# Kernel optimization log

Hardware: AMD Instinct MI355X
Metric: run time of the kernel (lower is better)

The kernel has to match this reference:

```python
import jax, jax.numpy as jnp
import numpy as np

N_VERTS = 2562


def _uniform(key, shape, bound):
    return jax.random.uniform(key, shape, jnp.float32, -bound, bound)


def vert_align(feat, pos):
    # feat: [B,C,H,W]; pos: [B,N,3], xy in [-1,1] -> bilinear sample -> [B,N,C]
    B, C, H, W = feat.shape
    ft = jnp.transpose(feat, (0, 2, 3, 1))  # [B,H,W,C]
    x = (jnp.clip(pos[..., 0], -1.0, 1.0) + 1.0) * 0.5 * (W - 1)
    y = (jnp.clip(pos[..., 1], -1.0, 1.0) + 1.0) * 0.5 * (H - 1)
    x0 = jnp.floor(x)
    y0 = jnp.floor(y)
    x0i = x0.astype(jnp.int32)
    y0i = y0.astype(jnp.int32)
    x1i = jnp.minimum(x0i + 1, W - 1)
    y1i = jnp.minimum(y0i + 1, H - 1)
    wx = (x - x0)[..., None]
    wy = (y - y0)[..., None]
    b = jnp.arange(B)[:, None]
    f00 = ft[b, y0i, x0i]
    f01 = ft[b, y0i, x1i]
    f10 = ft[b, y1i, x0i]
    f11 = ft[b, y1i, x1i]
    return (f00 * (1 - wx) * (1 - wy) + f01 * wx * (1 - wy)
            + f10 * (1 - wx) * wy + f11 * wx * wy)


def graph_conv(x, adj, w0, w1):
    # relu(x @ w0 + adj @ (x @ w1))
    return jax.nn.relu(x @ w0 + jnp.einsum('bij,bjc->bic', adj, x @ w1))


def setup_inputs() -> dict:
    key = jax.random.key(0)
    ks = jax.random.split(key, 20)
    B, N = 8, N_VERTS
    inp = {
        'conv2_3': jax.random.normal(ks[0], (B, 256, 56, 56), jnp.float32),
        'conv3_4': jax.random.normal(ks[1], (B, 512, 28, 28), jnp.float32),
        'conv4_6': jax.random.normal(ks[2], (B, 1024, 14, 14), jnp.float32),
        'conv5_3': jax.random.normal(ks[3], (B, 2048, 7, 7), jnp.float32),
        # scaled so row sums are O(1), like a normalized dense adjacency
        'vertex_adjacency': jax.random.uniform(ks[4], (B, N, N), jnp.float32) * (2.0 / N),
        'vertex_positions': jax.random.uniform(ks[5], (B, N, 3), jnp.float32) * 2.0 - 1.0,
        'vertex_features': jax.random.normal(ks[6], (B, N, 128), jnp.float32),
    }
    # learned parameters (torch default / GraphConv uniform init)
    inp['w_lin0'] = _uniform(ks[7], (3840, 128), 1.0 / np.sqrt(3840))
    inp['b_lin0'] = _uniform(ks[8], (128,), 1.0 / np.sqrt(3840))
    inp['gc0_w0'] = _uniform(ks[9], (259, 131), 1.0 / np.sqrt(259))
    inp['gc0_w1'] = _uniform(ks[10], (259, 131), 1.0 / np.sqrt(259))
    inp['gc1_w0'] = _uniform(ks[11], (131, 128), 1.0 / np.sqrt(131))
    inp['gc1_w1'] = _uniform(ks[12], (131, 128), 1.0 / np.sqrt(131))
    inp['gc2_w0'] = _uniform(ks[13], (131, 128), 1.0 / np.sqrt(131))
    inp['gc2_w1'] = _uniform(ks[14], (131, 128), 1.0 / np.sqrt(131))
    inp['w_lin1'] = _uniform(ks[15], (128, 3), 1.0 / np.sqrt(128))
    inp['b_lin1'] = _uniform(ks[16], (3,), 1.0 / np.sqrt(128))
    return inp


def reference(conv2_3, conv3_4, conv4_6, conv5_3, vertex_adjacency,
              vertex_positions, vertex_features,
              w_lin0, b_lin0, gc0_w0, gc0_w1, gc1_w0, gc1_w1,
              gc2_w0, gc2_w1, w_lin1, b_lin1):
    verts = jnp.concatenate(
        [vert_align(f, vertex_positions)
         for f in (conv2_3, conv3_4, conv4_6, conv5_3)], axis=2)  # [B,N,3840]
    projected = verts @ w_lin0 + b_lin0                             # [B,N,128]
    vf = jnp.concatenate([vertex_features, vertex_positions, projected], axis=2)  # 259
    h = graph_conv(vf, vertex_adjacency, gc0_w0, gc0_w1)            # [B,N,131]
    h = jnp.concatenate([vertex_positions, h], axis=2)              # 134? no: 3+131=134 -- see note
    h = graph_conv(h[:, :, :131] if h.shape[2] != 131 else h, vertex_adjacency, gc1_w0, gc1_w1)
    h = jnp.concatenate([vertex_positions, h], axis=2)              # 131
    new_features = graph_conv(h, vertex_adjacency, gc2_w0, gc2_w1)  # [B,N,128]
    new_positions = vertex_positions + jnp.tanh(new_features @ w_lin1 + b_lin1)
    return new_positions, new_features
```

## Files before the change

kernel.cpp:

```cpp
#include <hip/hip_runtime.h>
#include <hip/hip_bf16.h>

typedef __attribute__((ext_vector_type(8))) short bf16x8;
typedef __attribute__((ext_vector_type(4))) float f32x4;
typedef __attribute__((ext_vector_type(2))) float f32x2;
typedef long long i64;

static __device__ __forceinline__ float bflo(unsigned v){ return __uint_as_float(v << 16); }
static __device__ __forceinline__ float bfhi(unsigned v){ return __uint_as_float(v & 0xffff0000u); }
static __device__ __forceinline__ unsigned short f2bf(float f){
  unsigned u = __float_as_uint(f);
  u += 0x7FFFu + ((u >> 16) & 1u);
  return (unsigned short)(u >> 16);
}
static __device__ __forceinline__ unsigned f2e4m3(float x){
  unsigned b = __float_as_uint(x);
  unsigned s = (b >> 31) << 7;
  b &= 0x7fffffffu;
  if (b >= 0x43e80000u) return s | 0x7eu;
  if (b < 0x3c800000u)
    return s | (unsigned)rintf(__uint_as_float(b) * 512.f);
  unsigned b2 = b + 0x7ffffu + ((b >> 20) & 1u);
  return s | (((b2 >> 23) - 120u) << 3) | ((b2 >> 20) & 7u);
}
static __device__ __forceinline__ void gload_lds16(const void* g, void* l){
  __builtin_amdgcn_global_load_lds((const __attribute__((address_space(1))) unsigned int*)g,
                                   (__attribute__((address_space(3))) unsigned int*)l, 16, 0, 0);
}

#define MFMA16(acc, a, b) (acc) = __builtin_amdgcn_mfma_f32_16x16x32_bf16((a),(b),(acc),0,0,0)
#define MFMA8(acc, a, b)  (acc) = __builtin_amdgcn_mfma_f32_16x16x32_fp8_fp8((a),(b),(acc),0,0,0)

#define NB    8
#define NVRT  2562
#define MP    2624
#define NRB2  82
#define NRB16 164
#define NKT8  21
#define KOCT  336
#define YO    ((size_t)KOCT*128*8)

#define G_B0 0ul
#define G_B1 3211264ul
#define G_B2 4014080ul
#define G_B3 4214784ul
#define G_TOT 4264960ul

struct PWArgs {
  const float* src[7];
  unsigned short* dst[7];
  int ksrc[7], nsrc[7];
};
__global__ void k_packw_all(PWArgs a)
{
  const int cb[8] = {0,491520,528384,565248,585728,606208,626688,647168};
  int g = blockIdx.x * 256 + threadIdx.x;
#pragma unroll
  for (int s = 0; s < 7; s++){
    if (g >= cb[s] && g < cb[s+1]){
      int li = g - cb[s];
      int k = li >> 7, c = li & 127;
      int ks = a.ksrc[s], ns = a.nsrc[s];
      float v = (k < ks) ? a.src[s][(size_t)k * ns + c] : 0.f;
      a.dst[s][((size_t)(k >> 3) * 128 + c) * 8 + (k & 7)] = f2bf(v);
    }
  }
}

__global__ __launch_bounds__(256) void k_gproj2(
    const float* __restrict__ c0m, const float* __restrict__ c1m,
    const float* __restrict__ c2m, const float* __restrict__ c3m,
    const unsigned short* __restrict__ wp,
    unsigned short* __restrict__ G)
{
  __shared__ f32x4 red[3][1024];
  int bx = blockIdx.x;
  int m, b, tile;
  if (bx < 784)      { m = 0; b = bx / 98;  tile = bx - b*98; }
  else if (bx < 984) { int l = bx-784;  m = 1; b = l / 25; tile = l - b*25; }
  else if (bx < 1040){ int l = bx-984;  m = 2; b = l / 7;  tile = l - b*7; }
  else               { int l = bx-1040; m = 3; b = l >> 1; tile = l & 1; }
  int C  = 256 << m;
  int HW = (m==0)?3136:(m==1)?784:(m==2)?196:49;
  const float* src = ((m==0)?c0m:(m==1)?c1m:(m==2)?c2m:c3m) + (size_t)b * C * HW;
  size_t gb = ((m==0)?G_B0:(m==1)?G_B1:(m==2)?G_B2:G_B3) + (size_t)b * HW * 128;
  int ko8 = (m==0)?0:(m==1)?32:(m==2)?96:224;

  int t = threadIdx.x, w = t >> 6, lane = t & 63;
  int l15 = lane & 15, l4 = lane >> 4;
  int hw0 = tile * 32;
  int ar0 = min(hw0 + l15, HW - 1);
  int ar1 = min(hw0 + 16 + l15, HW - 1);

  f32x4 acc[2][8];
#pragma unroll
  for (int i = 0; i < 2; i++)
#pragma unroll
    for (int j = 0; j < 8; j++) acc[i][j] = (f32x4){0,0,0,0};

  int kq = C >> 2;
  int kbeg = w * kq, klim = kbeg + kq;
  for (int kb = kbeg; kb < klim; kb += 32){
    bf16x8 a0, a1;
#pragma unroll
    for (int j = 0; j < 8; j++){
      int cc = kb + l4*8 + j;
      a0[j] = (short)f2bf(src[(size_t)cc * HW + ar0]);
      a1[j] = (short)f2bf(src[(size_t)cc * HW + ar1]);
    }
    size_t bo = ((size_t)(ko8 + (kb>>3) + l4) * 128 + l15) * 8;
#pragma unroll
    for (int cf = 0; cf < 8; cf++){
      bf16x8 bb = *(const bf16x8*)(wp + bo + cf*128);
      MFMA16(acc[0][cf], a0, bb);
      MFMA16(acc[1][cf], a1, bb);
    }
  }

  if (w){
#pragma unroll
    for (int rf = 0; rf < 2; rf++)
#pragma unroll
      for (int cf = 0; cf < 8; cf++)
        red[w-1][(rf*8+cf)*64 + lane] = acc[rf][cf];
  }
  __syncthreads();
  if (!w){
#pragma unroll
    for (int rf = 0; rf < 2; rf++)
#pragma unroll
      for (int cf = 0; cf < 8; cf++){
        int i = (rf*8+cf)*64 + lane;
        f32x4 s = acc[rf][cf] + red[0][i] + red[1][i] + red[2][i];
        int col = cf*16 + l15;
#pragma unroll
        for (int r = 0; r < 4; r++){
          int hw = hw0 + rf*16 + l4*4 + r;
          if (hw < HW) G[gb + (size_t)hw*128 + col] = f2bf(s[r]);
        }
      }
  }
}

__global__ void k_prep2(const float* __restrict__ vfeat, const float* __restrict__ pos,
                        const unsigned short* __restrict__ G,
                        const float* __restrict__ bias,
                        unsigned short* __restrict__ vf,
                        unsigned short* __restrict__ x1,
                        unsigned short* __restrict__ x2,
                        unsigned char* __restrict__ y1A,
                        unsigned char* __restrict__ y1B)
{
  int b = blockIdx.y;
  if (blockIdx.x == 0){
    unsigned long long* za = (unsigned long long*)(y1A + (size_t)b*YO + (size_t)328*128*8);
    unsigned long long* zb = (unsigned long long*)(y1B + (size_t)b*YO + (size_t)328*128*8);
    int i = threadIdx.x;
#pragma unroll
    for (int j = 0; j < 4; j++){ za[i*4+j] = 0; zb[i*4+j] = 0; }
  }
  int row = blockIdx.x * 4 + (threadIdx.x >> 6);
  int lane = threadIdx.x & 63;
  size_t vfo = ((size_t)b * MP + row) * 288;
  size_t xo  = ((size_t)b * MP + row) * 160;
  if (row < NVRT){
    size_t src = (size_t)b * NVRT + row;
    float px = fminf(fmaxf(pos[src*3 + 0], -1.f), 1.f);
    float py = fminf(fmaxf(pos[src*3 + 1], -1.f), 1.f);
    int c0 = lane * 2;
    float s0 = bias[c0], s1 = bias[c0 + 1];
#pragma unroll
    for (int m = 0; m < 4; m++){
      int W = 56 >> m;
      int HW = W * W;
      size_t gb = (m==0)?G_B0:(m==1)?G_B1:(m==2)?G_B2:G_B3;
      float gx = (px + 1.f) * 0.5f * (float)(W - 1);
      float gy = (py + 1.f) * 0.5f * (float)(W - 1);
      int x0 = (int)floorf(gx), y0 = (int)floorf(gy);
      float wx = gx - (float)x0, wy = gy - (float)y0;
      int x1i = min(x0 + 1, W - 1), y1i = min(y0 + 1, W - 1);
      const unsigned short* g = G + gb + (size_t)b * HW * 128;
      unsigned v00 = *(const unsigned*)(g + ((size_t)(y0 *W + x0 ))*128 + c0);
      unsigned v01 = *(const unsigned*)(g + ((size_t)(y0 *W + x1i))*128 + c0);
      unsigned v10 = *(const unsigned*)(g + ((size_t)(y1i*W + x0 ))*128 + c0);
      unsigned v11 = *(const unsigned*)(g + ((size_t)(y1i*W + x1i))*128 + c0);
      float w00 = (1.f-wx)*(1.f-wy), w01 = wx*(1.f-wy);
      float w10 = (1.f-wx)*wy,       w11 = wx*wy;
      s0 += w00*bflo(v00) + w01*bflo(v01) + w10*bflo(v10) + w11*bflo(v11);
      s1 += w00*bfhi(v00) + w01*bfhi(v01) + w10*bfhi(v10) + w11*bfhi(v11);
    }
    vf[vfo + 131 + c0]     = f2bf(s0);
    vf[vfo + 131 + c0 + 1] = f2bf(s1);
    float2 fv = *(const float2*)(vfeat + src*128 + c0);
    vf[vfo + c0]     = f2bf(fv.x);
    vf[vfo + c0 + 1] = f2bf(fv.y);
    if (lane < 3){
      unsigned short v = f2bf(pos[src*3 + lane]);
      vf[vfo + 128 + lane] = v;
      x1[xo + lane] = v;
      x2[xo + lane] = v;
    }
    if (lane >= 32 && lane < 61) vf[vfo + 259 + (lane - 32)] = 0;
    if (lane < 29){ x1[xo + 131 + lane] = 0; x2[xo + 131 + lane] = 0; }
  } else {
    for (int c = lane; c < 288; c += 64) vf[vfo + c] = 0;
    for (int c = lane; c < 160; c += 64){ x1[xo + c] = 0; x2[xo + c] = 0; }
  }
}

__global__ void k_adjpack8(const float* __restrict__ adj, unsigned char* __restrict__ adjP)
{
  int kt = blockIdx.x, rb = blockIdx.y, b = blockIdx.z;
  int t = threadIdx.x;
  int r = t >> 4, kseg = t & 15;
  int grow = rb*16 + r, gk = kt*128 + kseg*8;
  float v[8];
  if (grow < NVRT && gk + 8 <= NVRT){
    const float4* p = (const float4*)(adj + ((size_t)b*NVRT + grow)*NVRT + gk);
    float4 f0 = p[0], f1 = p[1];
    v[0]=f0.x; v[1]=f0.y; v[2]=f0.z; v[3]=f0.w;
    v[4]=f1.x; v[5]=f1.y; v[6]=f1.z; v[7]=f1.w;
  } else if (grow < NVRT){
    const float* ap = adj + ((size_t)b*NVRT + grow)*NVRT;
#pragma unroll
    for (int e = 0; e < 8; e++){ int k = gk + e; v[e] = (k < NVRT) ? ap[k] : 0.f; }
  } else {
#pragma unroll
    for (int e = 0; e < 8; e++) v[e] = 0.f;
  }
  unsigned long long q = 0;
#pragma unroll
  for (int e = 0; e < 8; e++)
    q |= (unsigned long long)f2e4m3(v[e] * 1024.f) << (8*e);
  unsigned char* tb = adjP + (((size_t)b*NRB16 + rb)*NKT8 + kt) * 2048;
  *(unsigned long long*)(tb + 128*r + 8*(kseg ^ r)) = q;
}

template<int KX>
__global__ __launch_bounds__(256) void k_y1(
    const unsigned short* __restrict__ x,
    const unsigned short* __restrict__ wp1,
    unsigned char* __restrict__ y1p8)
{
  int b = blockIdx.y, rb = blockIdx.x * 32;
  int t = threadIdx.x, wave = t >> 6, lane = t & 63;
  int rf = wave & 1, ch = wave >> 1;
  int l15 = lane & 15, l4 = lane >> 4;
  f32x4 a1[4];
#pragma unroll
  for (int c = 0; c < 4; c++) a1[c] = (f32x4){0,0,0,0};
  int row = rb + rf*16 + l15;
  const unsigned short* xp = x + ((size_t)b * MP + row) * KX + l4 * 8;
#pragma unroll
  for (int kb = 0; kb < KX; kb += 32){
    bf16x8 a = *(const bf16x8*)(xp + kb);
    size_t bo = ((size_t)((kb>>3) + l4) * 128 + ch*64 + l15) * 8;
#pragma unroll
    for (int c = 0; c < 4; c++){
      bf16x8 b1 = *(const bf16x8*)(wp1 + bo + c*128);
      MFMA16(a1[c], a, b1);
    }
  }
  unsigned char* yb = y1p8 + (size_t)b * YO;
#pragma unroll
  for (int c = 0; c < 4; c++){
    int col = ch*64 + c*16 + l15;
    int orow0 = rb + rf*16 + l4*4;
    unsigned q = f2e4m3(a1[c][0]) | (f2e4m3(a1[c][1]) << 8)
               | (f2e4m3(a1[c][2]) << 16) | (f2e4m3(a1[c][3]) << 24);
    *(unsigned*)(yb + ((size_t)(orow0 >> 3) * 128 + col) * 8 + (orow0 & 7)) = q;
  }
}

template<int EPI, int KX>
__global__ __launch_bounds__(256) void k_adj8(
    const unsigned char* __restrict__ adjP,
    const unsigned char* __restrict__ y1in,
    const unsigned short* __restrict__ x,
    const unsigned short* __restrict__ wp0,
    const unsigned short* __restrict__ wp1n,
    unsigned char* __restrict__ y1out,
    const float* __restrict__ posg,
    unsigned short* __restrict__ xnext,
    float* __restrict__ outf,
    const float* __restrict__ wl1, const float* __restrict__ bl1,
    float* __restrict__ opos)
{
  __shared__ __align__(16) unsigned char abuf[2][2048];
  __shared__ unsigned short xbuf[EPI == 0 ? 16 : 1][168];
  __shared__ float hbuf[EPI == 1 ? 16 : 1][128];
  int rb = blockIdx.x, b = blockIdx.y;
  int t = threadIdx.x, w = t >> 6, lane = t & 63;
  int l15 = lane & 15, l4 = lane >> 4;
  const unsigned char* tb = adjP + (((size_t)b*NRB16 + rb)*NKT8) * 2048;
  const unsigned char* yb = y1in + (size_t)b * YO;

  f32x4 acc[2], accW[2];
  acc[0] = (f32x4){0,0,0,0};  acc[1] = (f32x4){0,0,0,0};
  accW[0] = (f32x4){0,0,0,0}; accW[1] = (f32x4){0,0,0,0};

  auto stage = [&](int kt, int bufi){
    if (w < 2)
      gload_lds16(tb + (size_t)kt*2048 + w*1024 + lane*16, &abuf[bufi][w*1024]);
  };

  stage(0, 0);

  if (EPI == 0){
    if (t < 48){
      int r16 = t / 3, c = t - r16*3;
      int grow = rb*16 + r16;
      xbuf[r16][c] = (grow < NVRT) ? f2bf(posg[((size_t)b*NVRT + grow)*3 + c]) : 0;
    }
    {
      int r16 = t >> 4, c0 = 131 + (t & 15);
      xbuf[r16][c0] = 0;
      if (c0 + 16 < 168) xbuf[r16][c0 + 16] = 0;
      if (c0 + 32 < 168) xbuf[r16][c0 + 32] = 0;
    }
  }

  const unsigned short* xr = x + ((size_t)b*MP + rb*16 + l15)*KX + l4*8;
#pragma unroll
  for (int kb = 0; kb < KX; kb += 32){
    bf16x8 ax = *(const bf16x8*)(xr + kb);
    size_t bo = ((size_t)((kb>>3) + l4)*128 + w*32 + l15)*8;
    MFMA16(accW[0], ax, *(const bf16x8*)(wp0 + bo));
    MFMA16(accW[1], ax, *(const bf16x8*)(wp0 + bo + 128));
  }

  __syncthreads();

  for (int kt = 0; kt < NKT8; ++kt){
    int cur = kt & 1;
    if (kt < NKT8-1) stage(kt+1, cur ^ 1);
    const unsigned char* ab = &abuf[cur][0];
#pragma unroll
    for (int sel = 0; sel < 2; sel++){
#pragma unroll
      for (int ks = 0; ks < 2; ks++){
        int koct = sel*8 + ks*4 + l4;
        i64 a = *(const i64*)(ab + 128*l15 + 8*(koct ^ l15));
        const unsigned char* bp = yb + ((size_t)(kt*16 + koct)*128 + w*32 + l15)*8;
        i64 b0 = *(const i64*)(bp);
        i64 b1 = *(const i64*)(bp + 128);
        MFMA8(acc[0], a, b0);
        MFMA8(acc[1], a, b1);
      }
    }
    __syncthreads();
  }

#pragma unroll
  for (int cf = 0; cf < 2; cf++){
    int col = w*32 + cf*16 + l15;
#pragma unroll
    for (int r = 0; r < 4; r++){
      int row16 = l4*4 + r;
      int row = rb*16 + row16;
      float v = fmaxf(accW[cf][r] + acc[cf][r] * 0.0009765625f, 0.f);
      if (EPI == 0){
        unsigned short hb = f2bf(v);
        if (row < NVRT) xnext[((size_t)b*MP + row)*160 + 3 + col] = hb;
        xbuf[row16][3 + col] = hb;
      } else {
        if (row < NVRT) outf[((size_t)b*NVRT + row)*128 + col] = v;
        hbuf[row16][col] = v;
      }
    }
  }
  __syncthreads();

  if (EPI == 0){
    f32x4 accY[2];
    accY[0] = (f32x4){0,0,0,0}; accY[1] = (f32x4){0,0,0,0};
#pragma unroll
    for (int ks = 0; ks < 5; ks++){
      bf16x8 a = *(const bf16x8*)(&xbuf[l15][ks*32 + l4*8]);
      size_t bo = ((size_t)(ks*4 + l4)*128 + w*32 + l15)*8;
      MFMA16(accY[0], a, *(const bf16x8*)(wp1n + bo));
      MFMA16(accY[1], a, *(const bf16x8*)(wp1n + bo + 128));
    }
    unsigned char* yo = y1out + (size_t)b * YO;
#pragma unroll
    for (int cf = 0; cf < 2; cf++){
      int col = w*32 + cf*16 + l15;
      int orow0 = rb*16 + l4*4;
      unsigned q = f2e4m3(accY[cf][0]) | (f2e4m3(accY[cf][1]) << 8)
                 | (f2e4m3(accY[cf][2]) << 16) | (f2e4m3(accY[cf][3]) << 24);
      *(unsigned*)(yo + ((size_t)(orow0 >> 3) * 128 + col) * 8 + (orow0 & 7)) = q;
    }
  } else {
#pragma unroll
    for (int rr = 0; rr < 4; rr++){
      int row16 = w*4 + rr;
      int grow = rb*16 + row16;
      if (grow < NVRT){
        int c0 = lane * 2;
        float v0 = hbuf[row16][c0], v1 = hbuf[row16][c0+1];
        float p[3];
#pragma unroll
        for (int j = 0; j < 3; j++){
          p[j] = v0 * wl1[c0*3 + j] + v1 * wl1[c0*3 + 3 + j];
#pragma unroll
          for (int off = 1; off < 64; off <<= 1)
            p[j] += __shfl_xor(p[j], off);
        }
        if (lane == 0){
          size_t po = ((size_t)b * NVRT + grow) * 3;
#pragma unroll
          for (int j = 0; j < 3; j++)
            opos[po + j] = posg[po + j] + tanhf(p[j] + bl1[j]);
        }
      }
    }
  }
}

extern "C" void kernel_launch(void* const* d_in, const int* in_sizes, int n_in,
                              void* d_out, int out_size, void* d_ws, size_t ws_size,
                              hipStream_t stream)
{
  const float* conv[4] = {(const float*)d_in[0], (const float*)d_in[1],
                          (const float*)d_in[2], (const float*)d_in[3]};
  const float* adj   = (const float*)d_in[4];
  const float* pos   = (const float*)d_in[5];
  const float* vfeat = (const float*)d_in[6];
  const float* wlin0 = (const float*)d_in[7];
  const float* blin0 = (const float*)d_in[8];
  const float* gw[6] = {(const float*)d_in[9],  (const float*)d_in[10],
                        (const float*)d_in[11], (const float*)d_in[12],
                        (const float*)d_in[13], (const float*)d_in[14]};
  const float* wlin1 = (const float*)d_in[15];
  const float* blin1 = (const float*)d_in[16];

  char* ws = (char*)d_ws;
  size_t off = 0;
  auto take = [&](size_t bytes)->char* {
    char* p = ws + off;
    off += (bytes + 255) & ~(size_t)255;
    return p;
  };
  unsigned short* G    = (unsigned short*)take(G_TOT * 2);
  unsigned char*  adjP = (unsigned char*)take((size_t)NB*NRB16*NKT8*2048);
  unsigned short* wl0p = (unsigned short*)take((size_t)3840*128*2);
  unsigned short* w0p0 = (unsigned short*)take((size_t)288*128*2);
  unsigned short* w1p0 = (unsigned short*)take((size_t)288*128*2);
  unsigned short* w0p1 = (unsigned short*)take((size_t)160*128*2);
  unsigned short* w1p1 = (unsigned short*)take((size_t)160*128*2);
  unsigned short* w0p2 = (unsigned short*)take((size_t)160*128*2);
  unsigned short* w1p2 = (unsigned short*)take((size_t)160*128*2);
  unsigned short* vf   = (unsigned short*)take((size_t)NB*MP*288*2);
  unsigned short* x1   = (unsigned short*)take((size_t)NB*MP*160*2);
  unsigned short* x2   = (unsigned short*)take((size_t)NB*MP*160*2);
  unsigned char*  y1A  = (unsigned char*)take((size_t)NB*YO);
  unsigned char*  y1B  = (unsigned char*)take((size_t)NB*YO);

  float* out_pos  = (float*)d_out;
  float* out_feat = out_pos + (size_t)NB*NVRT*3;

  PWArgs pw;
  pw.src[0]=wlin0; pw.dst[0]=wl0p; pw.ksrc[0]=3840; pw.nsrc[0]=128;
  pw.src[1]=gw[0]; pw.dst[1]=w0p0; pw.ksrc[1]=259;  pw.nsrc[1]=131;
  pw.src[2]=gw[1]; pw.dst[2]=w1p0; pw.ksrc[2]=259;  pw.nsrc[2]=131;
  pw.src[3]=gw[2]; pw.dst[3]=w0p1; pw.ksrc[3]=131;  pw.nsrc[3]=128;
  pw.src[4]=gw[3]; pw.dst[4]=w1p1; pw.ksrc[4]=131;  pw.nsrc[4]=128;
  pw.src[5]=gw[4]; pw.dst[5]=w0p2; pw.ksrc[5]=131;  pw.nsrc[5]=128;
  pw.src[6]=gw[5]; pw.dst[6]=w1p2; pw.ksrc[6]=131;  pw.nsrc[6]=128;
  k_packw_all<<<2528, 256, 0, stream>>>(pw);
  k_gproj2<<<1056, 256, 0, stream>>>(conv[0], conv[1], conv[2], conv[3], wl0p, G);
  k_prep2<<<dim3(MP/4, NB), 256, 0, stream>>>(vfeat, pos, G, blin0, vf, x1, x2, y1A, y1B);
  k_adjpack8<<<dim3(NKT8, NRB16, NB), 256, 0, stream>>>(adj, adjP);
  k_y1<288><<<dim3(NRB2, NB), 256, 0, stream>>>(vf, w1p0, y1A);
  k_adj8<0,288><<<dim3(NRB16, NB), 256, 0, stream>>>(adjP, y1A, vf, w0p0, w1p1, y1B, pos,
                                                     x1, nullptr, nullptr, nullptr, nullptr);
  k_adj8<0,160><<<dim3(NRB16, NB), 256, 0, stream>>>(adjP, y1B, x1, w0p1, w1p2, y1A, pos,
                                                     x2, nullptr, nullptr, nullptr, nullptr);
  k_adj8<1,160><<<dim3(NRB16, NB), 256, 0, stream>>>(adjP, y1A, x2, w0p2, nullptr, nullptr, pos,
                                                     nullptr, out_feat, wlin1, blin1, out_pos);
  (void)in_sizes; (void)n_in; (void)out_size; (void)ws_size;
}
```

Baseline: 262.2 us.

## Fuse fp32 adjacency fp8 packing into first graph-conv adjacency kernel

Removes the separate adjacency packing kernel and packs the fp32 adjacency to fp8 inside the first graph-conv kernel. Each row block reads its fp32 rows, converts them, stages them in shared memory for the MFMA, and writes the packed tiles to global memory for the later layers. This drops one launch and one re-read of the packed adjacency. In exchange the first layer's main loop becomes fp32-load bound, with only single-tile prefetch, and occupancy is limited to the row-block grid.

Result: no change. 261.0 us (-0.5%).

```diff
diff --git a/kernel.cpp b/kernel.cpp
--- a/kernel.cpp
+++ b/kernel.cpp
@@ -3,7 +3,6 @@
 
 typedef __attribute__((ext_vector_type(8))) short bf16x8;
 typedef __attribute__((ext_vector_type(4))) float f32x4;
-typedef __attribute__((ext_vector_type(2))) float f32x2;
 typedef long long i64;
 
 static __device__ __forceinline__ float bflo(unsigned v){ return __uint_as_float(v << 16); }
@@ -208,34 +207,6 @@
   }
 }
 
-__global__ void k_adjpack8(const float* __restrict__ adj, unsigned char* __restrict__ adjP)
-{
-  int kt = blockIdx.x, rb = blockIdx.y, b = blockIdx.z;
-  int t = threadIdx.x;
-  int r = t >> 4, kseg = t & 15;
-  int grow = rb*16 + r, gk = kt*128 + kseg*8;
-  float v[8];
-  if (grow < NVRT && gk + 8 <= NVRT){
-    const float4* p = (const float4*)(adj + ((size_t)b*NVRT + grow)*NVRT + gk);
-    float4 f0 = p[0], f1 = p[1];
-    v[0]=f0.x; v[1]=f0.y; v[2]=f0.z; v[3]=f0.w;
-    v[4]=f1.x; v[5]=f1.y; v[6]=f1.z; v[7]=f1.w;
-  } else if (grow < NVRT){
-    const float* ap = adj + ((size_t)b*NVRT + grow)*NVRT;
-#pragma unroll
-    for (int e = 0; e < 8; e++){ int k = gk + e; v[e] = (k < NVRT) ? ap[k] : 0.f; }
-  } else {
-#pragma unroll
-    for (int e = 0; e < 8; e++) v[e] = 0.f;
-  }
-  unsigned long long q = 0;
-#pragma unroll
-  for (int e = 0; e < 8; e++)
-    q |= (unsigned long long)f2e4m3(v[e] * 1024.f) << (8*e);
-  unsigned char* tb = adjP + (((size_t)b*NRB16 + rb)*NKT8 + kt) * 2048;
-  *(unsigned long long*)(tb + 128*r + 8*(kseg ^ r)) = q;
-}
-
 template<int KX>
 __global__ __launch_bounds__(256) void k_y1(
     const unsigned short* __restrict__ x,
@@ -269,6 +240,142 @@
     unsigned q = f2e4m3(a1[c][0]) | (f2e4m3(a1[c][1]) << 8)
                | (f2e4m3(a1[c][2]) << 16) | (f2e4m3(a1[c][3]) << 24);
     *(unsigned*)(yb + ((size_t)(orow0 >> 3) * 128 + col) * 8 + (orow0 & 7)) = q;
+  }
+}
+
+__global__ __launch_bounds__(256) void k_adjfuse(
+    const float* __restrict__ adj,
+    unsigned char* __restrict__ adjP,
+    const unsigned char* __restrict__ y1in,
+    const unsigned short* __restrict__ x,
+    const unsigned short* __restrict__ wp0,
+    const unsigned short* __restrict__ wp1n,
+    unsigned char* __restrict__ y1out,
+    const float* __restrict__ posg,
+    unsigned short* __restrict__ xnext)
+{
+  __shared__ __align__(16) unsigned char abuf[2][2048];
+  __shared__ unsigned short xbuf[16][168];
+  int rb = blockIdx.x, b = blockIdx.y;
+  int t = threadIdx.x, w = t >> 6, lane = t & 63;
+  int l15 = lane & 15, l4 = lane >> 4;
+  int r = t >> 4, kseg = t & 15;
+  int grow = rb*16 + r;
+  bool rv = grow < NVRT;
+  const float* arow = adj + ((size_t)b*NVRT + (rv ? grow : 0))*NVRT;
+  unsigned char* tb = adjP + (((size_t)b*NRB16 + rb)*NKT8) * 2048;
+  int tslot = 128*r + 8*(kseg ^ r);
+  const unsigned char* yb = y1in + (size_t)b * YO;
+
+  f32x4 acc[2], accW[2];
+  acc[0] = (f32x4){0,0,0,0};  acc[1] = (f32x4){0,0,0,0};
+  accW[0] = (f32x4){0,0,0,0}; accW[1] = (f32x4){0,0,0,0};
+
+  auto loadf32 = [&](int kt, float* v){
+    int gk = kt*128 + kseg*8;
+    if (rv && gk + 8 <= NVRT){
+      float4 f0 = *(const float4*)(arow + gk);
+      float4 f1 = *(const float4*)(arow + gk + 4);
+      v[0]=f0.x; v[1]=f0.y; v[2]=f0.z; v[3]=f0.w;
+      v[4]=f1.x; v[5]=f1.y; v[6]=f1.z; v[7]=f1.w;
+    } else if (rv){
+#pragma unroll
+      for (int e = 0; e < 8; e++){ int k = gk + e; v[e] = (k < NVRT) ? arow[k] : 0.f; }
+    } else {
+#pragma unroll
+      for (int e = 0; e < 8; e++) v[e] = 0.f;
+    }
+  };
+  auto cvt = [&](const float* v)->unsigned long long {
+    unsigned long long q = 0;
+#pragma unroll
+    for (int e = 0; e < 8; e++)
+      q |= (unsigned long long)f2e4m3(v[e] * 1024.f) << (8*e);
+    return q;
+  };
+
+  float v0[8];
+  loadf32(0, v0);
+
+  if (t < 48){
+    int r16 = t / 3, c = t - r16*3;
+    int g2 = rb*16 + r16;
+    xbuf[r16][c] = (g2 < NVRT) ? f2bf(posg[((size_t)b*NVRT + g2)*3 + c]) : 0;
+  }
+  {
+    int r16 = t >> 4, c0 = 131 + (t & 15);
+    xbuf[r16][c0] = 0;
+    if (c0 + 16 < 168) xbuf[r16][c0 + 16] = 0;
+    if (c0 + 32 < 168) xbuf[r16][c0 + 32] = 0;
+  }
+
+  const unsigned short* xr = x + ((size_t)b*MP + rb*16 + l15)*288 + l4*8;
+#pragma unroll
+  for (int kb = 0; kb < 288; kb += 32){
+    bf16x8 ax = *(const bf16x8*)(xr + kb);
+    size_t bo = ((size_t)((kb>>3) + l4)*128 + w*32 + l15)*8;
+    MFMA16(accW[0], ax, *(const bf16x8*)(wp0 + bo));
+    MFMA16(accW[1], ax, *(const bf16x8*)(wp0 + bo + 128));
+  }
+
+  unsigned long long q = cvt(v0);
+  float vn[8];
+
+  for (int kt = 0; kt < NKT8; ++kt){
+    int cur = kt & 1;
+    *(unsigned long long*)(&abuf[cur][tslot]) = q;
+    *(unsigned long long*)(tb + (size_t)kt*2048 + tslot) = q;
+    if (kt < NKT8-1) loadf32(kt+1, vn);
+    __syncthreads();
+    const unsigned char* ab = &abuf[cur][0];
+#pragma unroll
+    for (int sel = 0; sel < 2; sel++){
+#pragma unroll
+      for (int ks = 0; ks < 2; ks++){
+        int koct = sel*8 + ks*4 + l4;
+        i64 a = *(const i64*)(ab + 128*l15 + 8*(koct ^ l15));
+        const unsigned char* bp = yb + ((size_t)(kt*16 + koct)*128 + w*32 + l15)*8;
+        i64 b0 = *(const i64*)(bp);
+        i64 b1 = *(const i64*)(bp + 128);
+        MFMA8(acc[0], a, b0);
+        MFMA8(acc[1], a, b1);
+      }
+    }
+    if (kt < NKT8-1) q = cvt(vn);
+  }
+
+#pragma unroll
+  for (int cf = 0; cf < 2; cf++){
+    int col = w*32 + cf*16 + l15;
+#pragma unroll
+    for (int rr = 0; rr < 4; rr++){
+      int row16 = l4*4 + rr;
+      int row = rb*16 + row16;
+      float vv = fmaxf(accW[cf][rr] + acc[cf][rr] * 0.0009765625f, 0.f);
+      unsigned short hb = f2bf(vv);
+      if (row < NVRT) xnext[((size_t)b*MP + row)*160 + 3 + col] = hb;
+      xbuf[row16][3 + col] = hb;
+    }
+  }
+  __syncthreads();
+
+  f32x4 accY[2];
+  accY[0] = (f32x4){0,0,0,0}; accY[1] = (f32x4){0,0,0,0};
+#pragma unroll
+  for (int ks = 0; ks < 5; ks++){
+    bf16x8 a = *(const bf16x8*)(&xbuf[l15][ks*32 + l4*8]);
+    size_t bo = ((size_t)(ks*4 + l4)*128 + w*32 + l15)*8;
+    MFMA16(accY[0], a, *(const bf16x8*)(wp1n + bo));
+    MFMA16(accY[1], a, *(const bf16x8*)(wp1n + bo + 128));
+  }
+  unsigned char* yo = y1out + (size_t)b * YO;
+#pragma unroll
+  for (int cf = 0; cf < 2; cf++){
+    int col = w*32 + cf*16 + l15;
+    int orow0 = rb*16 + l4*4;
+    unsigned qq = f2e4m3(accY[cf][0]) | (f2e4m3(accY[cf][1]) << 8)
+                | (f2e4m3(accY[cf][2]) << 16) | (f2e4m3(accY[cf][3]) << 24);
+    *(unsigned*)(yo + ((size_t)(orow0 >> 3) * 128 + col) * 8 + (orow0 & 7)) = qq;
   }
 }
 
@@ -470,10 +577,8 @@
   k_packw_all<<<2528, 256, 0, stream>>>(pw);
   k_gproj2<<<1056, 256, 0, stream>>>(conv[0], conv[1], conv[2], conv[3], wl0p, G);
   k_prep2<<<dim3(MP/4, NB), 256, 0, stream>>>(vfeat, pos, G, blin0, vf, x1, x2, y1A, y1B);
-  k_adjpack8<<<dim3(NKT8, NRB16, NB), 256, 0, stream>>>(adj, adjP);
   k_y1<288><<<dim3(NRB2, NB), 256, 0, stream>>>(vf, w1p0, y1A);
-  k_adj8<0,288><<<dim3(NRB16, NB), 256, 0, stream>>>(adjP, y1A, vf, w0p0, w1p1, y1B, pos,
-                                                     x1, nullptr, nullptr, nullptr, nullptr);
+  k_adjfuse<<<dim3(NRB16, NB), 256, 0, stream>>>(adj, adjP, y1A, vf, w0p0, w1p1, y1B, pos, x1);
   k_adj8<0,160><<<dim3(NRB16, NB), 256, 0, stream>>>(adjP, y1B, x1, w0p1, w1p2, y1A, pos,
                                                      x2, nullptr, nullptr, nullptr, nullptr);
   k_adj8<1,160><<<dim3(NRB16, NB), 256, 0, stream>>>(adjP, y1A, x2, w0p2, nullptr, nullptr, pos,
```
